# Kernel optimization log

Measured on AMD Instinct MI355X. Metric: run time of the kernel, lower is better.

## Reference

```python
import jax, jax.numpy as jnp
import numpy as np

B, S, D, H = 2, 2048, 2048, 16
HD = D // H            # 128
HALF = HD // 2         # 64
SOFTCAP = 50.0
ROPE_BASE = 10000.0


def setup_inputs() -> dict:
    key = jax.random.key(0)
    k1, k2, k3 = jax.random.split(key, 3)
    inputs = jax.random.normal(k1, (B, S, D), dtype=jnp.float32)
    # param init ~ nnx.initializers.normal() (stddev 0.01 default; scale to keep activations sane)
    w_in = jax.random.normal(k2, (D, H, 3 * HD), dtype=jnp.float32) * (1.0 / np.sqrt(D))
    w_out = jax.random.normal(k3, (H, HD, D), dtype=jnp.float32) * (1.0 / np.sqrt(D))
    # RoPE tables: [S, HALF]
    pos = jnp.arange(S, dtype=jnp.float32)[:, None]
    inv_freq = 1.0 / (ROPE_BASE ** (jnp.arange(HALF, dtype=jnp.float32) / HALF))
    ang = pos * inv_freq[None, :]
    rope_sin = jnp.sin(ang)
    rope_cos = jnp.cos(ang)
    # causal mask [1, 1, S, S]
    mask = jnp.tril(jnp.ones((S, S), dtype=bool))[None, None, :, :]
    return {"inputs": inputs, "w_in": w_in, "w_out": w_out,
            "rope_sin": rope_sin, "rope_cos": rope_cos, "mask": mask}


def apply_rope(x, sin, cos):
    # x: [B, S, H, HD]; sin/cos: [S, HALF] -> broadcast [1, S, 1, HALF]
    sin = sin[None, :, None, :]
    cos = cos[None, :, None, :]
    x1, x2 = x[..., :HALF], x[..., HALF:]
    return jnp.concatenate([x1 * cos - x2 * sin, x2 * cos + x1 * sin], axis=-1)


def reference(inputs, w_in, w_out, rope_sin, rope_cos, mask):
    dtype = inputs.dtype
    # fused QKV projection: [B, S, H, 3*HD]
    qkv = jnp.einsum('bsd,bhf->bshf'.replace('bhf', 'dhf'), inputs, w_in)
    q, k, v = jnp.split(qkv, 3, axis=-1)           # each [B, S, H, HD]
    q = apply_rope(q, rope_sin, rope_cos)
    k = apply_rope(k, rope_sin, rope_cos)
    q = q / jnp.sqrt(jnp.asarray(HD, dtype))
    scores = jnp.einsum('bqhd,bkhd->bhqk', q, k)   # [B, H, S, S]
    big_neg = jnp.finfo(dtype).min
    scores = jnp.where(mask, scores, big_neg)
    scores = jnp.tanh(scores / SOFTCAP) * SOFTCAP  # softcap
    attn = jax.nn.softmax(scores, axis=-1)
    x = jnp.einsum('bhqk,bkhd->bqhd', attn, v)     # [B, S, H, HD]
    out = jnp.einsum('bqhd,hdm->bqm', x, w_out)    # [B, S, D]
    return out
```

## Files before the change

### kernel.cpp

```cpp
#include <hip/hip_runtime.h>

#define B_ 2
#define S_ 2048
#define D_ 2048
#define H_ 16
#define HD_ 128
#define NT_ (S_ / 64)

typedef unsigned short u16;
typedef __bf16 bf16x8 __attribute__((ext_vector_type(8)));
typedef float f32x4 __attribute__((ext_vector_type(4)));
typedef u16 u16x8 __attribute__((ext_vector_type(8)));

__device__ __forceinline__ float bf2f(u16 u) {
  unsigned int x = ((unsigned int)u) << 16;
  return __builtin_bit_cast(float, x);
}
__device__ __forceinline__ u16 f2bf(float f) {
  unsigned int u = __builtin_bit_cast(unsigned int, f);
  u += 0x7fffu + ((u >> 16) & 1u);
  return (u16)(u >> 16);
}
__device__ __forceinline__ void async16(const void* g, void* l) {
  __builtin_amdgcn_global_load_lds((const __attribute__((address_space(1))) void*)g,
                                   (__attribute__((address_space(3))) void*)l, 16, 0, 0);
}
__device__ __forceinline__ float vexp2(float x) {
  float r;
  asm("v_exp_f32 %0, %1" : "=v"(r) : "v"(x));
  return r;
}
__device__ __forceinline__ float vrcp(float x) {
  float r;
  asm("v_rcp_f32 %0, %1" : "=v"(r) : "v"(x));
  return r;
}

__global__ __launch_bounds__(256) void conv_f32_bf16(const float* __restrict__ in,
                                                     u16* __restrict__ outp, int n) {
  int idx = (blockIdx.x * 256 + threadIdx.x) * 4;
  int stride = gridDim.x * 256 * 4;
  for (; idx < n; idx += stride) {
    float4 v = *(const float4*)(in + idx);
    ushort4 ov = make_ushort4(f2bf(v.x), f2bf(v.y), f2bf(v.z), f2bf(v.w));
    *(ushort4*)(outp + idx) = ov;
  }
}

__global__ __launch_bounds__(256) void transpose_win(const float* __restrict__ in,
                                                     u16* __restrict__ outp) {
  __shared__ float tile[32][33];
  int n0 = blockIdx.x * 32, k0 = blockIdx.y * 32;
  int tx = threadIdx.x & 31, ty = threadIdx.x >> 5;
  int n = n0 + tx;
  int cc = n >> 7, p = n & 127;
  int q = (p >> 4) & 3;
  int d = ((p >> 6) << 5) + ((q >> 1) << 4) + ((q & 1) << 6) + (p & 15);
  int f = (cc / 3) * 384 + (cc % 3) * 128 + d;
#pragma unroll
  for (int yy = 0; yy < 32; yy += 8)
    tile[ty + yy][tx] = in[(size_t)(k0 + ty + yy) * 6144 + f];
  __syncthreads();
#pragma unroll
  for (int yy = 0; yy < 32; yy += 8)
    outp[(size_t)(n0 + ty + yy) * 2048 + k0 + tx] = f2bf(tile[tx][ty + yy]);
}

__global__ __launch_bounds__(256) void transpose_wout(const float* __restrict__ in,
                                                      u16* __restrict__ outp) {
  __shared__ float tile[32][33];
  int k0 = blockIdx.x * 32, n0 = blockIdx.y * 32;
  int tx = threadIdx.x & 31, ty = threadIdx.x >> 5;
#pragma unroll
  for (int yy = 0; yy < 32; yy += 8) {
    int kk = k0 + ty + yy;
    int hh = kk >> 7, j = kk & 127;
    int hd = (j & 7) * 16 + (j >> 3);
    tile[ty + yy][tx] = in[(size_t)(hh * 128 + hd) * 2048 + n0 + tx];
  }
  __syncthreads();
#pragma unroll
  for (int yy = 0; yy < 32; yy += 8)
    outp[(size_t)(n0 + ty + yy) * 2048 + k0 + tx] = f2bf(tile[tx][ty + yy]);
}

#define BAR __builtin_amdgcn_s_barrier()
#define LGKM0                                          \
  {                                                    \
    asm volatile("s_waitcnt lgkmcnt(0)" ::: "memory"); \
    __builtin_amdgcn_sched_barrier(0);                 \
  }
#define VM6 asm volatile("s_waitcnt vmcnt(6)" ::: "memory")
#define VM0 asm volatile("s_waitcnt vmcnt(0)" ::: "memory")
#define P1 __builtin_amdgcn_s_setprio(1)
#define P0 __builtin_amdgcn_s_setprio(0)

template <int EPI>
__global__ __launch_bounds__(512, 1) void gemm128(
    const u16* __restrict__ A, const u16* __restrict__ Bt, float* __restrict__ C, int K, int N,
    int ntn, u16* __restrict__ Qo, u16* __restrict__ Ko, u16* __restrict__ Vo,
    const float* __restrict__ rsin, const float* __restrict__ rcos) {
  __shared__ alignas(16) u16 lsA[3][128 * 64];
  __shared__ alignas(16) u16 lsB[3][256 * 64];
  const int tid = threadIdx.x;
  const int lane = tid & 63, wid = tid >> 6;
  const int g = lane >> 4, lr = lane & 15;
  const int wm = wid >> 2, wn = wid & 3;

  const int nwg = ntn << 5;
  const int bid = blockIdx.x;
  const int swz = (bid & 7) * (nwg >> 3) + (bid >> 3);
  const int m_idx = swz & 31, n_idx = swz >> 5;
  const size_t m0 = (size_t)m_idx * 128, n0 = (size_t)n_idx * 256;

  const int rowq = tid >> 3, slq = tid & 7;
  const int kofs = (slq ^ (rowq & 7)) << 3;
  const u16* pA0 = A + (m0 + rowq) * K + kofs;
  const u16* pA1 = A + (m0 + 64 + rowq) * K + kofs;
  const u16* pB0 = Bt + (n0 + rowq) * K + kofs;
  const u16* pB1 = Bt + (n0 + 64 + rowq) * K + kofs;
  const u16* pB2 = Bt + (n0 + 128 + rowq) * K + kofs;
  const u16* pB3 = Bt + (n0 + 192 + rowq) * K + kofs;

#define STG_A(t, buf)                                               \
  {                                                                 \
    async16(pA0 + (size_t)(t)*64, (char*)lsA[buf] + tid * 16);      \
    async16(pA1 + (size_t)(t)*64, (char*)lsA[buf] + 8192 + tid * 16); \
  }
#define STG_B(t, buf)                                                  \
  {                                                                    \
    async16(pB0 + (size_t)(t)*64, (char*)lsB[buf] + tid * 16);         \
    async16(pB1 + (size_t)(t)*64, (char*)lsB[buf] + 8192 + tid * 16);  \
    async16(pB2 + (size_t)(t)*64, (char*)lsB[buf] + 16384 + tid * 16); \
    async16(pB3 + (size_t)(t)*64, (char*)lsB[buf] + 24576 + tid * 16); \
  }

  const int sw0 = ((g) ^ (lr & 7)) << 4;
  const int sw1 = ((4 + g) ^ (lr & 7)) << 4;

#define LDA(tb)                                                              \
  {                                                                          \
    _Pragma("unroll") for (int i2 = 0; i2 < 4; ++i2) {                       \
      const char* _p = (const char*)lsA[tb] + (wm * 64 + i2 * 16 + lr) * 128; \
      aF[i2][0] = *(const bf16x8*)(_p + sw0);                                \
      aF[i2][1] = *(const bf16x8*)(_p + sw1);                                \
    }                                                                        \
  }
#define LDB(tb, dst, nh)                                                                \
  {                                                                                     \
    _Pragma("unroll") for (int j2 = 0; j2 < 2; ++j2) {                                  \
      const char* _p = (const char*)lsB[tb] + (wn * 64 + (nh)*32 + j2 * 16 + lr) * 128; \
      dst[j2][0] = *(const bf16x8*)(_p + sw0);                                          \
      dst[j2][1] = *(const bf16x8*)(_p + sw1);                                          \
    }                                                                                   \
  }
#define MM(nh, BB)                                                                           \
  {                                                                                          \
    _Pragma("unroll") for (int i2 = 0; i2 < 4; ++i2) _Pragma("unroll") for (int j2 = 0;     \
                                                                            j2 < 2; ++j2) { \
      acc[i2][(nh)*2 + j2] = __builtin_amdgcn_mfma_f32_16x16x32_bf16(                        \
          aF[i2][0], BB[j2][0], acc[i2][(nh)*2 + j2], 0, 0, 0);                              \
      acc[i2][(nh)*2 + j2] = __builtin_amdgcn_mfma_f32_16x16x32_bf16(                        \
          aF[i2][1], BB[j2][1], acc[i2][(nh)*2 + j2], 0, 0, 0);                              \
    }                                                                                        \
  }

  f32x4 acc[4][4] = {};
  const int nk = K >> 6;

  STG_A(0, 0);
  STG_B(0, 0);
  STG_A(1, 1);
  STG_B(1, 1);
  VM6;
  BAR;

  bf16x8 aF[4][2], b01[2][2], b23[2][2];
#pragma unroll 1
  for (int kt = 0; kt < nk; ++kt) {
    const int tb = kt % 3;
    const int sb = (kt + 2) % 3;
    const bool stg = (kt + 2) < nk;
    LDA(tb);
    LDB(tb, b01, 0);
    if (stg) STG_A(kt + 2, sb);
    BAR;
    LGKM0;
    P1;
    MM(0, b01);
    P0;
    BAR;
    LDB(tb, b23, 1);
    if (stg) STG_B(kt + 2, sb);
    BAR;
    LGKM0;
    P1;
    MM(1, b23);
    P0;
    if (kt < nk - 2) {
      VM6;
    } else {
      VM0;
    }
    BAR;
  }
#undef STG_A
#undef STG_B
#undef LDA
#undef LDB
#undef MM

  if (EPI == 0) {
#pragma unroll
    for (int i = 0; i < 4; ++i)
#pragma unroll
      for (int j = 0; j < 4; ++j)
#pragma unroll
        for (int r = 0; r < 4; ++r) {
          size_t m = m0 + wm * 64 + i * 16 + 4 * g + r;
          size_t n = n0 + wn * 64 + j * 16 + lr;
          C[m * N + n] = acc[i][j][r];
        }
  } else {
    const int c = (int)(n0 >> 7) + (wn >> 1);
    const int h = c / 3, part = c % 3;
    const int wn1 = wn & 1;
    if (part == 2) {
#pragma unroll
      for (int i = 0; i < 4; ++i) {
        int m = (int)m0 + wm * 64 + i * 16 + 4 * g;
        int b = m >> 11, s = m & (S_ - 1);
#pragma unroll
        for (int j = 0; j < 4; ++j) {
          int hd = wn1 * 32 + ((j >> 1) << 4) + ((j & 1) << 6) + lr;
          ushort4 pk;
          pk.x = f2bf(acc[i][j][0]);
          pk.y = f2bf(acc[i][j][1]);
          pk.z = f2bf(acc[i][j][2]);
          pk.w = f2bf(acc[i][j][3]);
          *(ushort4*)(Vo + ((size_t)(b * H_ + h) * HD_ + hd) * S_ + s) = pk;
        }
      }
    } else {
      u16* dstp = (part == 0) ? Qo : Ko;
      const float scl = (part == 0) ? 0.08838834764831845f : 1.0f;
#pragma unroll
      for (int i = 0; i < 4; ++i) {
        int mbase = (int)m0 + wm * 64 + i * 16 + 4 * g;
#pragma unroll
        for (int r = 0; r < 4; ++r) {
          int m = mbase + r;
          int b = m >> 11, s = m & (S_ - 1);
          const float* srow = rsin + s * 64;
          const float* crow = rcos + s * 64;
          u16* op = dstp + ((size_t)(b * H_ + h) * S_ + s) * HD_ + ((wn1 * 16 + lr) << 2);
          ushort4 pk;
          {
            int d = wn1 * 32 + lr;
            float cv = crow[d] * scl, sv = srow[d] * scl;
            float x1 = acc[i][0][r], x2 = acc[i][1][r];
            pk.x = f2bf(x1 * cv - x2 * sv);
            pk.y = f2bf(x2 * cv + x1 * sv);
          }
          {
            int d = wn1 * 32 + 16 + lr;
            float cv = crow[d] * scl, sv = srow[d] * scl;
            float x1 = acc[i][2][r], x2 = acc[i][3][r];
            pk.z = f2bf(x1 * cv - x2 * sv);
            pk.w = f2bf(x2 * cv + x1 * sv);
          }
          *(ushort4*)op = pk;
        }
      }
    }
  }
}

__global__ __launch_bounds__(256) void attn_fwd(const u16* __restrict__ Q, const u16* __restrict__ K,
                                                const u16* __restrict__ VT, u16* __restrict__ X) {
  const int bx = blockIdx.x;
  const int bh = blockIdx.y;
  const int tid = threadIdx.x;
  const int lane = tid & 63, wid = tid >> 6;
  const int g = lane >> 4, lr = lane & 15;

  __shared__ alignas(16) u16 lsK[2][64 * 128];
  __shared__ alignas(16) u16 lsV[2][128 * 64];
  __shared__ alignas(16) u16 lsP[4][16 * 72];

  const u16* Qp = Q + (size_t)bh * S_ * HD_;
  const u16* Kp = K + (size_t)bh * S_ * HD_;
  const u16* Vp = VT + (size_t)bh * HD_ * S_;
  u16* myP = lsP[wid];
  const int b = bh >> 4, h = bh & 15;

  const float c1 = -0.057707802f;
  const float c2 = -144.26950409f;

#pragma unroll 1
  for (int pass = 0; pass < 2; ++pass) {
    const int qt = pass ? bx : (NT_ - 1 - bx);
    const int qrow = qt * 64 + wid * 16 + lr;
    const int qbase = qt * 64 + wid * 16 + 4 * g;

    bf16x8 qf[4];
#pragma unroll
    for (int kc = 0; kc < 4; ++kc)
      qf[kc] = *(const bf16x8*)(Qp + (size_t)qrow * HD_ + kc * 32 + g * 8);

    f32x4 o[8] = {};
    float psum[4] = {0.f, 0.f, 0.f, 0.f};

#pragma unroll
    for (int p = 0; p < 4; ++p) {
      int c = p * 256 + tid;
      int rowk = c >> 4;
      int wsk = ((c & 15) << 4) ^ ((rowk & 7) << 4);
      async16((const char*)Kp + (((size_t)rowk) << 8) + wsk, (char*)lsK[0] + c * 16);
      int rowv = c >> 3;
      int wsv = ((c & 7) << 4) ^ ((rowv & 7) << 4);
      async16((const char*)Vp + (size_t)rowv * (S_ * 2) + wsv, (char*)lsV[0] + c * 16);
    }
    __syncthreads();

    int cur = 0;
    for (int kt = 0; kt <= qt; ++kt) {
      if (kt < qt) {
        const int nxt = kt + 1;
#pragma unroll
        for (int p = 0; p < 4; ++p) {
          int c = p * 256 + tid;
          int rowk = c >> 4;
          int wsk = ((c & 15) << 4) ^ ((rowk & 7) << 4);
          async16((const char*)Kp + (((size_t)(nxt * 64 + rowk)) << 8) + wsk,
                  (char*)lsK[cur ^ 1] + c * 16);
          int rowv = c >> 3;
          int wsv = ((c & 7) << 4) ^ ((rowv & 7) << 4);
          async16((const char*)Vp + (size_t)rowv * (S_ * 2) + nxt * 128 + wsv,
                  (char*)lsV[cur ^ 1] + c * 16);
        }
      }
      f32x4 sc[4];
#pragma unroll
      for (int jn = 0; jn < 4; ++jn) {
        f32x4 a = {0.f, 0.f, 0.f, 0.f};
        const int row = jn * 16 + lr;
        const int sw = (row & 7) << 4;
#pragma unroll
        for (int kc = 0; kc < 4; ++kc) {
          int w = (kc * 64 + g * 16) ^ sw;
          bf16x8 kf = *(const bf16x8*)((const char*)lsK[cur] + row * 256 + w);
          a = __builtin_amdgcn_mfma_f32_16x16x32_bf16(qf[kc], kf, a, 0, 0, 0);
        }
        sc[jn] = a;
      }
#pragma unroll
      for (int jn = 0; jn < 4; ++jn) {
        int key = kt * 64 + jn * 16 + lr;
#pragma unroll
        for (int r = 0; r < 4; ++r) {
          float z = vexp2(c1 * sc[jn][r]);
          float p = vexp2(c2 * z * vrcp(1.f + z));
          if (key > qbase + r) p = 0.f;
          psum[r] += p;
          myP[(4 * g + r) * 72 + jn * 16 + lr] = f2bf(p);
        }
      }
#pragma unroll
      for (int kc = 0; kc < 2; ++kc) {
        bf16x8 pa = *(const bf16x8*)(myP + lr * 72 + kc * 32 + g * 8);
#pragma unroll
        for (int jh = 0; jh < 8; ++jh) {
          int row = jh * 16 + lr;
          int w = (kc * 64 + g * 16) ^ ((row & 7) << 4);
          bf16x8 vf = *(const bf16x8*)((const char*)lsV[cur] + row * 128 + w);
          o[jh] = __builtin_amdgcn_mfma_f32_16x16x32_bf16(pa, vf, o[jh], 0, 0, 0);
        }
      }
      __syncthreads();
      cur ^= 1;
    }
    float lsum[4];
#pragma unroll
    for (int r = 0; r < 4; ++r) {
      float s = psum[r];
#pragma unroll
      for (int msk = 1; msk < 16; msk <<= 1) s += __shfl_xor(s, msk, 64);
      lsum[r] = s;
    }
#pragma unroll
    for (int r = 0; r < 4; ++r) {
      float inv = 1.f / lsum[r];
      int s = qbase + r;
      u16x8 pk;
#pragma unroll
      for (int jh = 0; jh < 8; ++jh) pk[jh] = f2bf(o[jh][r] * inv);
      *(u16x8*)(X + ((size_t)(b * S_ + s)) * D_ + h * HD_ + lr * 8) = pk;
    }
  }
}

extern "C" void kernel_launch(void* const* d_in, const int* in_sizes, int n_in,
                              void* d_out, int out_size, void* d_ws, size_t ws_size,
                              hipStream_t stream) {
  const float* inputs = (const float*)d_in[0];
  const float* w_in = (const float*)d_in[1];
  const float* w_out = (const float*)d_in[2];
  const float* rsin = (const float*)d_in[3];
  const float* rcos = (const float*)d_in[4];
  float* out = (float*)d_out;

  char* ws = (char*)d_ws;
  u16* bfA = (u16*)(ws);
  u16* w_inT = (u16*)(ws + 16777216);
  u16* Qraw = (u16*)(ws + 41943040);
  u16* Kraw = (u16*)(ws + 58720256);
  u16* VT = (u16*)(ws + 75497472);
  u16* Xbuf = (u16*)(ws);
  u16* w_outT = (u16*)(ws + 16777216);

  conv_f32_bf16<<<2048, 256, 0, stream>>>(inputs, bfA, B_ * S_ * D_);
  transpose_win<<<dim3(192, 64), 256, 0, stream>>>(w_in, w_inT);
  gemm128<1><<<768, 512, 0, stream>>>(bfA, w_inT, nullptr, 2048, 6144, 24, Qraw, Kraw, VT,
                                      rsin, rcos);
  transpose_wout<<<dim3(64, 64), 256, 0, stream>>>(w_out, w_outT);
  attn_fwd<<<dim3(NT_ / 2, 32), 256, 0, stream>>>(Qraw, Kraw, VT, Xbuf);
  gemm128<0><<<256, 512, 0, stream>>>(Xbuf, w_outT, out, 2048, 2048, 8,
                                      nullptr, nullptr, nullptr, nullptr, nullptr);
}
```

Baseline: 278.3 us.

## Switch projection GEMM to 32x32x16 MFMA tiles with a single barrier phase

Rewrites the shared GEMM kernel to use 32x32x16 bf16 MFMA instructions with 2x2 accumulator tiles per wave instead of 4x4 tiles of 16x16x32. All A/B fragments for a k-step are loaded at once, which removes the split into two half-steps and the extra barriers between them. The w_in column permutation and the QKV/RoPE epilogue are rederived for the new accumulator layout. The aim is fewer LDS reads per flop and less synchronization, at the cost of more live registers and narrower ushort2 stores in the Q/K epilogue.

```diff
diff --git a/kernel.cpp b/kernel.cpp
--- a/kernel.cpp
+++ b/kernel.cpp
@@ -10,6 +10,7 @@
 typedef unsigned short u16;
 typedef __bf16 bf16x8 __attribute__((ext_vector_type(8)));
 typedef float f32x4 __attribute__((ext_vector_type(4)));
+typedef float f32x16 __attribute__((ext_vector_type(16)));
 typedef u16 u16x8 __attribute__((ext_vector_type(8)));
 
 __device__ __forceinline__ float bf2f(u16 u) {
@@ -54,8 +55,7 @@
   int tx = threadIdx.x & 31, ty = threadIdx.x >> 5;
   int n = n0 + tx;
   int cc = n >> 7, p = n & 127;
-  int q = (p >> 4) & 3;
-  int d = ((p >> 6) << 5) + ((q >> 1) << 4) + ((q & 1) << 6) + (p & 15);
+  int d = ((p >> 6) << 5) + (((p >> 5) & 1) << 6) + (p & 31);
   int f = (cc / 3) * 384 + (cc % 3) * 128 + d;
 #pragma unroll
   for (int yy = 0; yy < 32; yy += 8)
@@ -104,7 +104,7 @@
   __shared__ alignas(16) u16 lsB[3][256 * 64];
   const int tid = threadIdx.x;
   const int lane = tid & 63, wid = tid >> 6;
-  const int g = lane >> 4, lr = lane & 15;
+  const int c31 = lane & 31, hh = lane >> 5;
   const int wm = wid >> 2, wn = wid & 3;
 
   const int nwg = ntn << 5;
@@ -122,9 +122,9 @@
   const u16* pB2 = Bt + (n0 + 128 + rowq) * K + kofs;
   const u16* pB3 = Bt + (n0 + 192 + rowq) * K + kofs;
 
-#define STG_A(t, buf)                                               \
-  {                                                                 \
-    async16(pA0 + (size_t)(t)*64, (char*)lsA[buf] + tid * 16);      \
+#define STG_A(t, buf)                                                 \
+  {                                                                   \
+    async16(pA0 + (size_t)(t)*64, (char*)lsA[buf] + tid * 16);        \
     async16(pA1 + (size_t)(t)*64, (char*)lsA[buf] + 8192 + tid * 16); \
   }
 #define STG_B(t, buf)                                                  \
@@ -135,37 +135,18 @@
     async16(pB3 + (size_t)(t)*64, (char*)lsB[buf] + 24576 + tid * 16); \
   }
 
-  const int sw0 = ((g) ^ (lr & 7)) << 4;
-  const int sw1 = ((4 + g) ^ (lr & 7)) << 4;
-
-#define LDA(tb)                                                              \
-  {                                                                          \
-    _Pragma("unroll") for (int i2 = 0; i2 < 4; ++i2) {                       \
-      const char* _p = (const char*)lsA[tb] + (wm * 64 + i2 * 16 + lr) * 128; \
-      aF[i2][0] = *(const bf16x8*)(_p + sw0);                                \
-      aF[i2][1] = *(const bf16x8*)(_p + sw1);                                \
-    }                                                                        \
-  }
-#define LDB(tb, dst, nh)                                                                \
-  {                                                                                     \
-    _Pragma("unroll") for (int j2 = 0; j2 < 2; ++j2) {                                  \
-      const char* _p = (const char*)lsB[tb] + (wn * 64 + (nh)*32 + j2 * 16 + lr) * 128; \
-      dst[j2][0] = *(const bf16x8*)(_p + sw0);                                          \
-      dst[j2][1] = *(const bf16x8*)(_p + sw1);                                          \
-    }                                                                                   \
-  }
-#define MM(nh, BB)                                                                           \
-  {                                                                                          \
-    _Pragma("unroll") for (int i2 = 0; i2 < 4; ++i2) _Pragma("unroll") for (int j2 = 0;     \
-                                                                            j2 < 2; ++j2) { \
-      acc[i2][(nh)*2 + j2] = __builtin_amdgcn_mfma_f32_16x16x32_bf16(                        \
-          aF[i2][0], BB[j2][0], acc[i2][(nh)*2 + j2], 0, 0, 0);                              \
-      acc[i2][(nh)*2 + j2] = __builtin_amdgcn_mfma_f32_16x16x32_bf16(                        \
-          aF[i2][1], BB[j2][1], acc[i2][(nh)*2 + j2], 0, 0, 0);                              \
-    }                                                                                        \
-  }
-
-  f32x4 acc[4][4] = {};
+  int ofsA[2][4], ofsB[2][4];
+#pragma unroll
+  for (int mi = 0; mi < 2; ++mi)
+#pragma unroll
+    for (int t = 0; t < 4; ++t) {
+      int ra = wm * 64 + mi * 32 + c31;
+      ofsA[mi][t] = ra * 128 + (((t * 2 + hh) ^ (c31 & 7)) << 4);
+      int rb = wn * 64 + mi * 32 + c31;
+      ofsB[mi][t] = rb * 128 + (((t * 2 + hh) ^ (c31 & 7)) << 4);
+    }
+
+  f32x16 acc[2][2] = {};
   const int nk = K >> 6;
 
   STG_A(0, 0);
@@ -175,27 +156,36 @@
   VM6;
   BAR;
 
-  bf16x8 aF[4][2], b01[2][2], b23[2][2];
 #pragma unroll 1
   for (int kt = 0; kt < nk; ++kt) {
     const int tb = kt % 3;
     const int sb = (kt + 2) % 3;
     const bool stg = (kt + 2) < nk;
-    LDA(tb);
-    LDB(tb, b01, 0);
-    if (stg) STG_A(kt + 2, sb);
-    BAR;
+    bf16x8 aF[2][4], bF[2][4];
+#pragma unroll
+    for (int mi = 0; mi < 2; ++mi)
+#pragma unroll
+      for (int t = 0; t < 4; ++t)
+        aF[mi][t] = *(const bf16x8*)((const char*)lsA[tb] + ofsA[mi][t]);
+#pragma unroll
+    for (int ni = 0; ni < 2; ++ni)
+#pragma unroll
+      for (int t = 0; t < 4; ++t)
+        bF[ni][t] = *(const bf16x8*)((const char*)lsB[tb] + ofsB[ni][t]);
+    if (stg) {
+      STG_A(kt + 2, sb);
+      STG_B(kt + 2, sb);
+    }
     LGKM0;
     P1;
-    MM(0, b01);
-    P0;
-    BAR;
-    LDB(tb, b23, 1);
-    if (stg) STG_B(kt + 2, sb);
-    BAR;
-    LGKM0;
-    P1;
-    MM(1, b23);
+#pragma unroll
+    for (int t = 0; t < 4; ++t)
+#pragma unroll
+      for (int mi = 0; mi < 2; ++mi)
+#pragma unroll
+        for (int ni = 0; ni < 2; ++ni)
+          acc[mi][ni] =
+              __builtin_amdgcn_mfma_f32_32x32x16_bf16(aF[mi][t], bF[ni][t], acc[mi][ni], 0, 0, 0);
     P0;
     if (kt < nk - 2) {
       VM6;
@@ -206,20 +196,17 @@
   }
 #undef STG_A
 #undef STG_B
-#undef LDA
-#undef LDB
-#undef MM
 
   if (EPI == 0) {
 #pragma unroll
-    for (int i = 0; i < 4; ++i)
-#pragma unroll
-      for (int j = 0; j < 4; ++j)
-#pragma unroll
-        for (int r = 0; r < 4; ++r) {
-          size_t m = m0 + wm * 64 + i * 16 + 4 * g + r;
-          size_t n = n0 + wn * 64 + j * 16 + lr;
-          C[m * N + n] = acc[i][j][r];
+    for (int mi = 0; mi < 2; ++mi)
+#pragma unroll
+      for (int ni = 0; ni < 2; ++ni)
+#pragma unroll
+        for (int reg = 0; reg < 16; ++reg) {
+          size_t m = m0 + wm * 64 + mi * 32 + (reg & 3) + 8 * (reg >> 2) + 4 * hh;
+          size_t n = n0 + wn * 64 + ni * 32 + c31;
+          C[m * N + n] = acc[mi][ni][reg];
         }
   } else {
     const int c = (int)(n0 >> 7) + (wn >> 1);
@@ -227,51 +214,40 @@
     const int wn1 = wn & 1;
     if (part == 2) {
 #pragma unroll
-      for (int i = 0; i < 4; ++i) {
-        int m = (int)m0 + wm * 64 + i * 16 + 4 * g;
-        int b = m >> 11, s = m & (S_ - 1);
-#pragma unroll
-        for (int j = 0; j < 4; ++j) {
-          int hd = wn1 * 32 + ((j >> 1) << 4) + ((j & 1) << 6) + lr;
-          ushort4 pk;
-          pk.x = f2bf(acc[i][j][0]);
-          pk.y = f2bf(acc[i][j][1]);
-          pk.z = f2bf(acc[i][j][2]);
-          pk.w = f2bf(acc[i][j][3]);
-          *(ushort4*)(Vo + ((size_t)(b * H_ + h) * HD_ + hd) * S_ + s) = pk;
-        }
-      }
+      for (int mi = 0; mi < 2; ++mi)
+#pragma unroll
+        for (int ni = 0; ni < 2; ++ni) {
+          int hd = wn1 * 32 + c31 + 64 * ni;
+#pragma unroll
+          for (int rq = 0; rq < 4; ++rq) {
+            int m = (int)m0 + wm * 64 + mi * 32 + 8 * rq + 4 * hh;
+            int b = m >> 11, s = m & (S_ - 1);
+            ushort4 pk;
+            pk.x = f2bf(acc[mi][ni][rq * 4 + 0]);
+            pk.y = f2bf(acc[mi][ni][rq * 4 + 1]);
+            pk.z = f2bf(acc[mi][ni][rq * 4 + 2]);
+            pk.w = f2bf(acc[mi][ni][rq * 4 + 3]);
+            *(ushort4*)(Vo + ((size_t)(b * H_ + h) * HD_ + hd) * S_ + s) = pk;
+          }
+        }
     } else {
       u16* dstp = (part == 0) ? Qo : Ko;
       const float scl = (part == 0) ? 0.08838834764831845f : 1.0f;
-#pragma unroll
-      for (int i = 0; i < 4; ++i) {
-        int mbase = (int)m0 + wm * 64 + i * 16 + 4 * g;
-#pragma unroll
-        for (int r = 0; r < 4; ++r) {
-          int m = mbase + r;
+      const int d = wn1 * 32 + c31;
+      const int jofs = c31 * 4 + wn1 * 2;
+#pragma unroll
+      for (int mi = 0; mi < 2; ++mi)
+#pragma unroll
+        for (int reg = 0; reg < 16; ++reg) {
+          int m = (int)m0 + wm * 64 + mi * 32 + (reg & 3) + 8 * (reg >> 2) + 4 * hh;
           int b = m >> 11, s = m & (S_ - 1);
-          const float* srow = rsin + s * 64;
-          const float* crow = rcos + s * 64;
-          u16* op = dstp + ((size_t)(b * H_ + h) * S_ + s) * HD_ + ((wn1 * 16 + lr) << 2);
-          ushort4 pk;
-          {
-            int d = wn1 * 32 + lr;
-            float cv = crow[d] * scl, sv = srow[d] * scl;
-            float x1 = acc[i][0][r], x2 = acc[i][1][r];
-            pk.x = f2bf(x1 * cv - x2 * sv);
-            pk.y = f2bf(x2 * cv + x1 * sv);
-          }
-          {
-            int d = wn1 * 32 + 16 + lr;
-            float cv = crow[d] * scl, sv = srow[d] * scl;
-            float x1 = acc[i][2][r], x2 = acc[i][3][r];
-            pk.z = f2bf(x1 * cv - x2 * sv);
-            pk.w = f2bf(x2 * cv + x1 * sv);
-          }
-          *(ushort4*)op = pk;
-        }
-      }
+          float cv = rcos[s * 64 + d] * scl, sv = rsin[s * 64 + d] * scl;
+          float x1 = acc[mi][0][reg], x2 = acc[mi][1][reg];
+          ushort2 pk;
+          pk.x = f2bf(x1 * cv - x2 * sv);
+          pk.y = f2bf(x2 * cv + x1 * sv);
+          *(ushort2*)(dstp + ((size_t)(b * H_ + h) * S_ + s) * HD_ + jofs) = pk;
+        }
     }
   }
 }
```

Measured after the change: 278.2 us. About the same (-0.0%).
